# Kernel tuning notes

Hardware: AMD Instinct MI355X
Metric: run time of the kernel (lower is better)

Reference implementation:

```python
import jax, jax.numpy as jnp
import numpy as np

H = 16
D_MODEL = 1024
D_K = D_MODEL // H  # 64


def setup_inputs() -> dict:
    key = jax.random.key(0)
    ks = jax.random.split(key, 8)
    B, S = 8, 1024
    q = jax.random.normal(ks[0], (B, S, D_MODEL), dtype=jnp.float32)
    k = jax.random.normal(ks[1], (B, S, D_MODEL), dtype=jnp.float32)
    v = jax.random.normal(ks[2], (B, S, D_MODEL), dtype=jnp.float32)
    # xavier_normal for [h, d_model, d_k]: std = sqrt(2 / (d_model + d_k)) (fan over last two dims)
    std_p = float(np.sqrt(2.0 / (D_MODEL + D_K)))
    W_q = jax.random.normal(ks[3], (H, D_MODEL, D_K), dtype=jnp.float32) * std_p
    W_k = jax.random.normal(ks[4], (H, D_MODEL, D_K), dtype=jnp.float32) * std_p
    W_v = jax.random.normal(ks[5], (H, D_MODEL, D_K), dtype=jnp.float32) * std_p
    std_o = float(np.sqrt(2.0 / (H * D_K + D_MODEL)))
    W_o = jax.random.normal(ks[6], (D_MODEL, H * D_K), dtype=jnp.float32) * std_o  # torch Linear weight [out, in]
    b_o = jax.random.normal(ks[7], (D_MODEL,), dtype=jnp.float32) * 0.01
    return {"q": q, "k": k, "v": v, "W_q": W_q, "W_k": W_k, "W_v": W_v, "W_o": W_o, "b_o": b_o}


def reference(q, k, v, W_q, W_k, W_v, W_o, b_o):
    B, S, _ = q.shape
    # per-head projections: [h, b, s, d_k]
    qh = jnp.einsum('bsd,hdk->hbsk', q, W_q)
    kh = jnp.einsum('bsd,hdk->hbsk', k, W_k)
    vh = jnp.einsum('bsd,hdk->hbsk', v, W_v)
    scale = 1.0 / jnp.sqrt(jnp.asarray(D_K, dtype=q.dtype))
    scores = jnp.einsum('hbsk,hbtk->hbst', qh, kh) * scale  # [h,b,s,s]
    attn = jax.nn.softmax(scores, axis=-1)
    c = jnp.einsum('hbst,hbtk->hbsk', attn, vh)  # [h,b,s,d_k]
    # torch code splits the stacked (h*b) batch and concats on feature dim:
    # head index becomes the OUTER factor of the feature dim -> [b,s,h*d_k]
    c = jnp.transpose(c, (1, 2, 0, 3)).reshape(B, S, H * D_K)
    out = c @ W_o.T + b_o
    return out
```

## Files before the change

### kernel.cpp

```cpp
#include <hip/hip_runtime.h>
#include <hip/hip_bf16.h>

typedef __bf16 bf16_t;
typedef __attribute__((ext_vector_type(8))) __bf16 bf16x8;
typedef __attribute__((ext_vector_type(4))) float f32x4;

#define MFMA(a, b, c) __builtin_amdgcn_mfma_f32_16x16x32_bf16(a, b, c, 0, 0, 0)

__device__ inline void gload_lds16(const bf16_t* g, bf16_t* l) {
  __builtin_amdgcn_global_load_lds(
      (const __attribute__((address_space(1))) void*)g,
      (__attribute__((address_space(3))) void*)l, 16, 0, 0);
}

__global__ void fill_sentinel(float* out, int n, float val) {
  int i = blockIdx.x * blockDim.x + threadIdx.x;
  if (i < n) out[i] = val;
}

__global__ void transpose_w(const float* __restrict__ Wq, const float* __restrict__ Wk,
                            const float* __restrict__ Wv, bf16_t* __restrict__ Wt) {
  int gid = blockIdx.x * blockDim.x + threadIdx.x;
  int e = gid * 8;
  int m = e >> 20;
  int rem = e & 1048575;
  int n = rem >> 10;
  int d0 = rem & 1023;
  const float* W = (m == 0) ? Wq : (m == 1) ? Wk : Wv;
  int h = n >> 6, kk = n & 63;
  union { bf16_t h8[8]; uint4 u; } tmp;
#pragma unroll
  for (int j = 0; j < 8; ++j)
    tmp.h8[j] = (bf16_t)W[((size_t)(h * 1024 + d0 + j)) * 64 + kk];
  *(uint4*)(Wt + e) = tmp.u;
}

__global__ void cvt_bf16(const float* __restrict__ in, bf16_t* __restrict__ out) {
  size_t i = (size_t)(blockIdx.x * blockDim.x + threadIdx.x) * 8;
  f32x4 a = *(const f32x4*)(in + i);
  f32x4 b = *(const f32x4*)(in + i + 4);
  bf16x8 r;
  r[0] = (bf16_t)a[0]; r[1] = (bf16_t)a[1]; r[2] = (bf16_t)a[2]; r[3] = (bf16_t)a[3];
  r[4] = (bf16_t)b[0]; r[5] = (bf16_t)b[1]; r[6] = (bf16_t)b[2]; r[7] = (bf16_t)b[3];
  *(bf16x8*)(out + i) = r;
}

template <int MODE>
__global__ void gemm_bt(const bf16_t* __restrict__ A, const bf16_t* __restrict__ Bt,
                        const float* __restrict__ bias, void* __restrict__ out_,
                        int M, int N, int K, float scale) {
  __shared__ bf16_t sA[2][128 * 32];
  __shared__ bf16_t sB[2][128 * 32];
  const int t = threadIdx.x;
  const int w = t >> 6, l = t & 63;
  const int lq = l >> 4, ll = l & 15;
  const int m0 = blockIdx.x * 128, n0 = blockIdx.y * 128;
  const int wr = (w >> 1) * 64, wc = (w & 1) * 64;
  const int srow = l >> 2;
  const int scol = (l & 3) * 8;
  f32x4 acc[4][4] = {};

  auto stage = [&](int bufi, int k0s) {
#pragma unroll
    for (int c = 0; c < 2; ++c) {
      int ch = w * 2 + c;
      int row = ch * 16 + srow;
      gload_lds16(A  + (size_t)(m0 + row) * K + k0s + scol, sA[bufi] + ch * 512);
      gload_lds16(Bt + (size_t)(n0 + row) * K + k0s + scol, sB[bufi] + ch * 512);
    }
  };

  stage(0, 0);
  __syncthreads();

  int cur = 0;
  for (int k0 = 0; k0 < K; k0 += 32) {
    if (k0 + 32 < K) stage(cur ^ 1, k0 + 32);
    bf16x8 af[4], bfr[4];
#pragma unroll
    for (int i = 0; i < 4; ++i) {
      af[i]  = *(const bf16x8*)(sA[cur] + (wr + i * 16 + ll) * 32 + lq * 8);
      bfr[i] = *(const bf16x8*)(sB[cur] + (wc + i * 16 + ll) * 32 + lq * 8);
    }
#pragma unroll
    for (int mi = 0; mi < 4; ++mi)
#pragma unroll
      for (int ni = 0; ni < 4; ++ni)
        acc[mi][ni] = MFMA(af[mi], bfr[ni], acc[mi][ni]);
    __syncthreads();
    cur ^= 1;
  }
#pragma unroll
  for (int mi = 0; mi < 4; ++mi)
#pragma unroll
    for (int ni = 0; ni < 4; ++ni)
#pragma unroll
      for (int r = 0; r < 4; ++r) {
        int row = m0 + wr + mi * 16 + lq * 4 + r;
        int col = n0 + wc + ni * 16 + ll;
        float v = acc[mi][ni][r];
        if (MODE == 2) {
          ((float*)out_)[(size_t)row * N + col] = v + bias[col];
        } else {
          int h = col >> 6, kk = col & 63, b = row >> 10, s = row & 1023;
          size_t idx;
          if (MODE == 0)
            idx = ((size_t)((h * 8 + b) * 1024 + s)) * 64 + kk;
          else
            idx = ((size_t)((h * 8 + b) * 64 + kk)) * 1024 + s;
          ((bf16_t*)out_)[idx] = (bf16_t)(v * scale);
        }
      }
}

__global__ void attn_kernel(const bf16_t* __restrict__ qh, const bf16_t* __restrict__ kh,
                            const bf16_t* __restrict__ vt, bf16_t* __restrict__ c) {
  constexpr int KP = 72, PP = 72;
  __shared__ bf16_t sK[2][64 * KP];
  __shared__ bf16_t sP[4][16 * PP];
  const int t = threadIdx.x;
  const int w = t >> 6, l = t & 63;
  const int lq = l >> 4, ll = l & 15;
  const int orig = blockIdx.x + (blockIdx.y << 4);
  const int wg = (orig & 7) * 256 + (orig >> 3);
  const int q0 = (wg & 15) * 64;
  const int hb = wg >> 4;
  const int h = hb >> 3, b = hb & 7;
  const size_t base = (size_t)hb * 65536;
  const bf16_t* Q = qh + base + (size_t)q0 * 64;
  const bf16_t* K = kh + base;
  const bf16_t* V = vt + base;

  bf16x8 aq0 = *(const bf16x8*)(Q + (w * 16 + ll) * 64 + 0 * 32 + lq * 8);
  bf16x8 aq1 = *(const bf16x8*)(Q + (w * 16 + ll) * 64 + 1 * 32 + lq * 8);

  {
    int e0 = t * 8, e1 = (256 + t) * 8;
    uint4 ka = *(const uint4*)(K + e0);
    uint4 kb = *(const uint4*)(K + e1);
    *(uint4*)(sK[0] + (e0 >> 6) * KP + (e0 & 63)) = ka;
    *(uint4*)(sK[0] + (e1 >> 6) * KP + (e1 & 63)) = kb;
  }
  __syncthreads();

  float mrow = -1e30f, lrow = 0.f;
  f32x4 o[4] = {};
  bf16_t* Pw = sP[w];

  int cur = 0;
  for (int kt = 0; kt < 1024; kt += 64, cur ^= 1) {
    uint4 kr0, kr1;
    if (kt < 960) {
      kr0 = *(const uint4*)(K + (size_t)(kt + 64) * 64 + t * 8);
      kr1 = *(const uint4*)(K + (size_t)(kt + 64) * 64 + (256 + t) * 8);
    }
    const bf16_t* Vb = V + (size_t)ll * 1024 + kt + lq * 8;
    bf16x8 bv00 = *(const bf16x8*)(Vb + 0 * 16384 + 0);
    bf16x8 bv01 = *(const bf16x8*)(Vb + 1 * 16384 + 0);
    bf16x8 bv02 = *(const bf16x8*)(Vb + 2 * 16384 + 0);
    bf16x8 bv03 = *(const bf16x8*)(Vb + 3 * 16384 + 0);
    bf16x8 bv10 = *(const bf16x8*)(Vb + 0 * 16384 + 32);
    bf16x8 bv11 = *(const bf16x8*)(Vb + 1 * 16384 + 32);
    bf16x8 bv12 = *(const bf16x8*)(Vb + 2 * 16384 + 32);
    bf16x8 bv13 = *(const bf16x8*)(Vb + 3 * 16384 + 32);

    f32x4 sacc[4] = {};
    __builtin_amdgcn_s_setprio(1);
#pragma unroll
    for (int ni = 0; ni < 4; ++ni) {
      bf16x8 bk0 = *(const bf16x8*)(sK[cur] + (ni * 16 + ll) * KP + 0 * 32 + lq * 8);
      bf16x8 bk1 = *(const bf16x8*)(sK[cur] + (ni * 16 + ll) * KP + 1 * 32 + lq * 8);
      sacc[ni] = MFMA(bk0, aq0, sacc[ni]);
      sacc[ni] = MFMA(bk1, aq1, sacc[ni]);
    }
    __builtin_amdgcn_s_setprio(0);
    float rmax = -1e30f;
#pragma unroll
    for (int ni = 0; ni < 4; ++ni)
#pragma unroll
      for (int r = 0; r < 4; ++r)
        rmax = fmaxf(rmax, sacc[ni][r]);
    if (!__all(rmax <= mrow + 8.0f)) {
      rmax = fmaxf(rmax, __shfl_xor(rmax, 16));
      rmax = fmaxf(rmax, __shfl_xor(rmax, 32));
      float mnew = fmaxf(mrow, rmax);
      float alpha = __expf(mrow - mnew);
      mrow = mnew;
      lrow *= alpha;
#pragma unroll
      for (int r = 0; r < 4; ++r) {
        float ar = __shfl(alpha, lq * 4 + r, 16);
#pragma unroll
        for (int ni = 0; ni < 4; ++ni)
          o[ni][r] *= ar;
      }
    }
#pragma unroll
    for (int ni = 0; ni < 4; ++ni)
#pragma unroll
      for (int r = 0; r < 4; ++r) {
        float p = __expf(sacc[ni][r] - mrow);
        sacc[ni][r] = p;
        lrow += p;
      }
#pragma unroll
    for (int ni = 0; ni < 4; ++ni) {
      union { bf16_t h4[4]; uint2 u; } pk;
      pk.h4[0] = (bf16_t)sacc[ni][0];
      pk.h4[1] = (bf16_t)sacc[ni][1];
      pk.h4[2] = (bf16_t)sacc[ni][2];
      pk.h4[3] = (bf16_t)sacc[ni][3];
      *(uint2*)(Pw + ll * PP + ni * 16 + lq * 4) = pk.u;
    }
    asm volatile("s_waitcnt lgkmcnt(0)" ::: "memory");
    __builtin_amdgcn_sched_barrier(0);
    bf16x8 ap0 = *(const bf16x8*)(Pw + ll * PP + 0 * 32 + lq * 8);
    bf16x8 ap1 = *(const bf16x8*)(Pw + ll * PP + 1 * 32 + lq * 8);
    __builtin_amdgcn_s_setprio(1);
    o[0] = MFMA(ap0, bv00, o[0]);
    o[1] = MFMA(ap0, bv01, o[1]);
    o[2] = MFMA(ap0, bv02, o[2]);
    o[3] = MFMA(ap0, bv03, o[3]);
    o[0] = MFMA(ap1, bv10, o[0]);
    o[1] = MFMA(ap1, bv11, o[1]);
    o[2] = MFMA(ap1, bv12, o[2]);
    o[3] = MFMA(ap1, bv13, o[3]);
    __builtin_amdgcn_s_setprio(0);
    if (kt < 960) {
      int e0 = t * 8, e1 = (256 + t) * 8;
      *(uint4*)(sK[cur ^ 1] + (e0 >> 6) * KP + (e0 & 63)) = kr0;
      *(uint4*)(sK[cur ^ 1] + (e1 >> 6) * KP + (e1 & 63)) = kr1;
    }
    __syncthreads();
  }
  lrow += __shfl_xor(lrow, 16);
  lrow += __shfl_xor(lrow, 32);
#pragma unroll
  for (int r = 0; r < 4; ++r) {
    float lr = __shfl(lrow, lq * 4 + r, 16);
    int s = q0 + w * 16 + lq * 4 + r;
#pragma unroll
    for (int ni = 0; ni < 4; ++ni) {
      int dk = ni * 16 + ll;
      c[((size_t)(b * 1024 + s)) * 1024 + h * 64 + dk] = (bf16_t)(o[ni][r] / lr);
    }
  }
}

extern "C" void kernel_launch(void* const* d_in, const int* in_sizes, int n_in,
                              void* d_out, int out_size, void* d_ws, size_t ws_size,
                              hipStream_t stream) {
  float* out = (float*)d_out;
  int nblk_out = (out_size + 255) / 256;
  if (n_in != 8) {
    fill_sentinel<<<nblk_out, 256, 0, stream>>>(out, out_size, 600.0f + 10.0f * n_in);
    return;
  }
  const int expect[8] = {8388608, 8388608, 8388608, 1048576,
                         1048576, 1048576, 1048576, 1024};
  for (int i = 0; i < 8; ++i)
    if (in_sizes[i] != expect[i]) {
      fill_sentinel<<<nblk_out, 256, 0, stream>>>(out, out_size, 500.0f + 10.0f * i);
      return;
    }

  bf16_t* ws   = (bf16_t*)d_ws;
  bf16_t* qhb  = ws;
  bf16_t* khb  = ws + 8388608;
  bf16_t* vtb  = ws + 16777216;
  bf16_t* Wt   = ws + 25165824;
  bf16_t* cbuf = ws + 25165824;
  bf16_t* Wob  = ws;
  if (ws_size < 67108864ull) {
    fill_sentinel<<<nblk_out, 256, 0, stream>>>(out, out_size, 400.0f);
    return;
  }

  const float* q  = (const float*)d_in[0];
  const float* k  = (const float*)d_in[1];
  const float* v  = (const float*)d_in[2];
  const float* Wq = (const float*)d_in[3];
  const float* Wk = (const float*)d_in[4];
  const float* Wv = (const float*)d_in[5];
  const float* Wo = (const float*)d_in[6];
  const float* bo = (const float*)d_in[7];

  bf16_t* qb = (bf16_t*)d_out;
  bf16_t* kb = (bf16_t*)d_out + 8388608;
  bf16_t* vb = (bf16_t*)d_out;

  transpose_w<<<1536, 256, 0, stream>>>(Wq, Wk, Wv, Wt);
  cvt_bf16<<<4096, 256, 0, stream>>>(q, qb);
  cvt_bf16<<<4096, 256, 0, stream>>>(k, kb);
  dim3 gg(64, 8);
  gemm_bt<0><<<gg, 256, 0, stream>>>(qb, Wt,           nullptr, qhb, 8192, 1024, 1024, 0.125f);
  gemm_bt<0><<<gg, 256, 0, stream>>>(kb, Wt + 1048576, nullptr, khb, 8192, 1024, 1024, 1.0f);
  cvt_bf16<<<4096, 256, 0, stream>>>(v, vb);
  gemm_bt<1><<<gg, 256, 0, stream>>>(vb, Wt + 2097152, nullptr, vtb, 8192, 1024, 1024, 1.0f);
  attn_kernel<<<dim3(16, 128), 256, 0, stream>>>(qhb, khb, vtb, cbuf);
  cvt_bf16<<<512, 256, 0, stream>>>(Wo, Wob);
  gemm_bt<2><<<gg, 256, 0, stream>>>(cbuf, Wob, bo, out, 8192, 1024, 1024, 1.0f);
}
```

Measured before the change: 412.5 us.

## Load K fragments directly from global memory and drop LDS staging and barriers

Each wave now reads its K tile straight from global memory into registers instead of staging it cooperatively into double-buffered shared memory. This removes the per-iteration block-wide __syncthreads and the LDS writes and reads for K, which frees the four waves to run independently. The cost is that each of the four waves loads the same K tile separately, so global/L2 traffic for K goes up fourfold. The K loads are also no longer prefetched one iteration ahead, so their latency now sits directly before the QK MFMAs.

New measurement: 511.7 us. 24.0% more time.

```diff
diff --git a/kernel.cpp b/kernel.cpp
--- a/kernel.cpp
+++ b/kernel.cpp
@@ -115,8 +115,7 @@
 
 __global__ void attn_kernel(const bf16_t* __restrict__ qh, const bf16_t* __restrict__ kh,
                             const bf16_t* __restrict__ vt, bf16_t* __restrict__ c) {
-  constexpr int KP = 72, PP = 72;
-  __shared__ bf16_t sK[2][64 * KP];
+  constexpr int PP = 72;
   __shared__ bf16_t sP[4][16 * PP];
   const int t = threadIdx.x;
   const int w = t >> 6, l = t & 63;
@@ -134,26 +133,33 @@
   bf16x8 aq0 = *(const bf16x8*)(Q + (w * 16 + ll) * 64 + 0 * 32 + lq * 8);
   bf16x8 aq1 = *(const bf16x8*)(Q + (w * 16 + ll) * 64 + 1 * 32 + lq * 8);
 
-  {
-    int e0 = t * 8, e1 = (256 + t) * 8;
-    uint4 ka = *(const uint4*)(K + e0);
-    uint4 kb = *(const uint4*)(K + e1);
-    *(uint4*)(sK[0] + (e0 >> 6) * KP + (e0 & 63)) = ka;
-    *(uint4*)(sK[0] + (e1 >> 6) * KP + (e1 & 63)) = kb;
-  }
-  __syncthreads();
-
   float mrow = -1e30f, lrow = 0.f;
   f32x4 o[4] = {};
   bf16_t* Pw = sP[w];
 
-  int cur = 0;
-  for (int kt = 0; kt < 1024; kt += 64, cur ^= 1) {
-    uint4 kr0, kr1;
-    if (kt < 960) {
-      kr0 = *(const uint4*)(K + (size_t)(kt + 64) * 64 + t * 8);
-      kr1 = *(const uint4*)(K + (size_t)(kt + 64) * 64 + (256 + t) * 8);
-    }
+  for (int kt = 0; kt < 1024; kt += 64) {
+    const bf16_t* Kb = K + (size_t)(kt + ll) * 64 + lq * 8;
+    bf16x8 bk00 = *(const bf16x8*)(Kb + 0 * 1024 + 0);
+    bf16x8 bk01 = *(const bf16x8*)(Kb + 1 * 1024 + 0);
+    bf16x8 bk02 = *(const bf16x8*)(Kb + 2 * 1024 + 0);
+    bf16x8 bk03 = *(const bf16x8*)(Kb + 3 * 1024 + 0);
+    bf16x8 bk10 = *(const bf16x8*)(Kb + 0 * 1024 + 32);
+    bf16x8 bk11 = *(const bf16x8*)(Kb + 1 * 1024 + 32);
+    bf16x8 bk12 = *(const bf16x8*)(Kb + 2 * 1024 + 32);
+    bf16x8 bk13 = *(const bf16x8*)(Kb + 3 * 1024 + 32);
+
+    f32x4 sacc[4] = {};
+    __builtin_amdgcn_s_setprio(1);
+    sacc[0] = MFMA(bk00, aq0, sacc[0]);
+    sacc[1] = MFMA(bk01, aq0, sacc[1]);
+    sacc[2] = MFMA(bk02, aq0, sacc[2]);
+    sacc[3] = MFMA(bk03, aq0, sacc[3]);
+    sacc[0] = MFMA(bk10, aq1, sacc[0]);
+    sacc[1] = MFMA(bk11, aq1, sacc[1]);
+    sacc[2] = MFMA(bk12, aq1, sacc[2]);
+    sacc[3] = MFMA(bk13, aq1, sacc[3]);
+    __builtin_amdgcn_s_setprio(0);
+
     const bf16_t* Vb = V + (size_t)ll * 1024 + kt + lq * 8;
     bf16x8 bv00 = *(const bf16x8*)(Vb + 0 * 16384 + 0);
     bf16x8 bv01 = *(const bf16x8*)(Vb + 1 * 16384 + 0);
@@ -164,16 +170,6 @@
     bf16x8 bv12 = *(const bf16x8*)(Vb + 2 * 16384 + 32);
     bf16x8 bv13 = *(const bf16x8*)(Vb + 3 * 16384 + 32);
 
-    f32x4 sacc[4] = {};
-    __builtin_amdgcn_s_setprio(1);
-#pragma unroll
-    for (int ni = 0; ni < 4; ++ni) {
-      bf16x8 bk0 = *(const bf16x8*)(sK[cur] + (ni * 16 + ll) * KP + 0 * 32 + lq * 8);
-      bf16x8 bk1 = *(const bf16x8*)(sK[cur] + (ni * 16 + ll) * KP + 1 * 32 + lq * 8);
-      sacc[ni] = MFMA(bk0, aq0, sacc[ni]);
-      sacc[ni] = MFMA(bk1, aq1, sacc[ni]);
-    }
-    __builtin_amdgcn_s_setprio(0);
     float rmax = -1e30f;
 #pragma unroll
     for (int ni = 0; ni < 4; ++ni)
@@ -226,12 +222,6 @@
     o[2] = MFMA(ap1, bv12, o[2]);
     o[3] = MFMA(ap1, bv13, o[3]);
     __builtin_amdgcn_s_setprio(0);
-    if (kt < 960) {
-      int e0 = t * 8, e1 = (256 + t) * 8;
-      *(uint4*)(sK[cur ^ 1] + (e0 >> 6) * KP + (e0 & 63)) = kr0;
-      *(uint4*)(sK[cur ^ 1] + (e1 >> 6) * KP + (e1 & 63)) = kr1;
-    }
-    __syncthreads();
   }
   lrow += __shfl_xor(lrow, 16);
   lrow += __shfl_xor(lrow, 32);
```

## Merge Q and K projection GEMMs into one launch and shrink GEMM M-tile to 64

Applied to the files above, without the earlier changes.

The GEMM tile changes from 128x128 to 64x128, with each wave now covering a 64x32 slice, so every GEMM launches twice as many workgroups and fills more CUs. The Q and K projections become a single launch over 16384 rows, choosing the weight slice and scale from the row offset, since qb and kb lie next to each other in memory. The goal is less launch overhead and better occupancy. In exchange each workgroup reuses the B tile less and does more LDS loads per MFMA.

Measured after the change: 421.2 us. 2.1% more time.

```diff
diff --git a/kernel.cpp b/kernel.cpp
--- a/kernel.cpp
+++ b/kernel.cpp
@@ -46,27 +46,28 @@
 }
 
 template <int MODE>
-__global__ void gemm_bt(const bf16_t* __restrict__ A, const bf16_t* __restrict__ Bt,
-                        const float* __restrict__ bias, void* __restrict__ out_,
-                        int M, int N, int K, float scale) {
-  __shared__ bf16_t sA[2][128 * 32];
+__global__ void gemm_bt(const bf16_t* __restrict__ A, const bf16_t* __restrict__ Bt_,
+                        const float* __restrict__ bias, void* __restrict__ out_) {
+  __shared__ bf16_t sA[2][64 * 32];
   __shared__ bf16_t sB[2][128 * 32];
   const int t = threadIdx.x;
   const int w = t >> 6, l = t & 63;
   const int lq = l >> 4, ll = l & 15;
-  const int m0 = blockIdx.x * 128, n0 = blockIdx.y * 128;
-  const int wr = (w >> 1) * 64, wc = (w & 1) * 64;
+  const int m0 = blockIdx.x * 64, n0 = blockIdx.y * 128;
+  const bf16_t* Bt = (MODE == 0 && m0 >= 8192) ? Bt_ + 1048576 : Bt_;
+  const float scale = (MODE == 0 && m0 < 8192) ? 0.125f : 1.0f;
   const int srow = l >> 2;
   const int scol = (l & 3) * 8;
-  f32x4 acc[4][4] = {};
+  f32x4 acc[4][2] = {};
 
   auto stage = [&](int bufi, int k0s) {
+    gload_lds16(A + (size_t)(m0 + w * 16 + srow) * 1024 + k0s + scol,
+                sA[bufi] + w * 512);
 #pragma unroll
     for (int c = 0; c < 2; ++c) {
       int ch = w * 2 + c;
-      int row = ch * 16 + srow;
-      gload_lds16(A  + (size_t)(m0 + row) * K + k0s + scol, sA[bufi] + ch * 512);
-      gload_lds16(Bt + (size_t)(n0 + row) * K + k0s + scol, sB[bufi] + ch * 512);
+      gload_lds16(Bt + (size_t)(n0 + ch * 16 + srow) * 1024 + k0s + scol,
+                  sB[bufi] + ch * 512);
     }
   };
 
@@ -74,18 +75,19 @@
   __syncthreads();
 
   int cur = 0;
-  for (int k0 = 0; k0 < K; k0 += 32) {
-    if (k0 + 32 < K) stage(cur ^ 1, k0 + 32);
-    bf16x8 af[4], bfr[4];
-#pragma unroll
-    for (int i = 0; i < 4; ++i) {
-      af[i]  = *(const bf16x8*)(sA[cur] + (wr + i * 16 + ll) * 32 + lq * 8);
-      bfr[i] = *(const bf16x8*)(sB[cur] + (wc + i * 16 + ll) * 32 + lq * 8);
-    }
+  for (int k0 = 0; k0 < 1024; k0 += 32) {
+    if (k0 + 32 < 1024) stage(cur ^ 1, k0 + 32);
+    bf16x8 af[4], bfr[2];
+#pragma unroll
+    for (int i = 0; i < 4; ++i)
+      af[i] = *(const bf16x8*)(sA[cur] + (i * 16 + ll) * 32 + lq * 8);
+#pragma unroll
+    for (int i = 0; i < 2; ++i)
+      bfr[i] = *(const bf16x8*)(sB[cur] + (w * 32 + i * 16 + ll) * 32 + lq * 8);
 #pragma unroll
     for (int mi = 0; mi < 4; ++mi)
 #pragma unroll
-      for (int ni = 0; ni < 4; ++ni)
+      for (int ni = 0; ni < 2; ++ni)
         acc[mi][ni] = MFMA(af[mi], bfr[ni], acc[mi][ni]);
     __syncthreads();
     cur ^= 1;
@@ -93,21 +95,22 @@
 #pragma unroll
   for (int mi = 0; mi < 4; ++mi)
 #pragma unroll
-    for (int ni = 0; ni < 4; ++ni)
+    for (int ni = 0; ni < 2; ++ni)
 #pragma unroll
       for (int r = 0; r < 4; ++r) {
-        int row = m0 + wr + mi * 16 + lq * 4 + r;
-        int col = n0 + wc + ni * 16 + ll;
+        int row = m0 + mi * 16 + lq * 4 + r;
+        int col = n0 + w * 32 + ni * 16 + ll;
         float v = acc[mi][ni][r];
         if (MODE == 2) {
-          ((float*)out_)[(size_t)row * N + col] = v + bias[col];
+          ((float*)out_)[(size_t)row * 1024 + col] = v + bias[col];
+        } else if (MODE == 1) {
+          int h = col >> 6, kk = col & 63, b = row >> 10, s = row & 1023;
+          ((bf16_t*)out_)[((size_t)((h * 8 + b) * 64 + kk)) * 1024 + s] = (bf16_t)v;
         } else {
-          int h = col >> 6, kk = col & 63, b = row >> 10, s = row & 1023;
-          size_t idx;
-          if (MODE == 0)
-            idx = ((size_t)((h * 8 + b) * 1024 + s)) * 64 + kk;
-          else
-            idx = ((size_t)((h * 8 + b) * 64 + kk)) * 1024 + s;
+          int mat = row >> 13, rr = row & 8191;
+          int h = col >> 6, kk = col & 63, b = rr >> 10, s = rr & 1023;
+          size_t idx = (size_t)mat * 8388608 +
+                       ((size_t)((h * 8 + b) * 1024 + s)) * 64 + kk;
           ((bf16_t*)out_)[idx] = (bf16_t)(v * scale);
         }
       }
@@ -266,7 +269,6 @@
 
   bf16_t* ws   = (bf16_t*)d_ws;
   bf16_t* qhb  = ws;
-  bf16_t* khb  = ws + 8388608;
   bf16_t* vtb  = ws + 16777216;
   bf16_t* Wt   = ws + 25165824;
   bf16_t* cbuf = ws + 25165824;
@@ -292,12 +294,10 @@
   transpose_w<<<1536, 256, 0, stream>>>(Wq, Wk, Wv, Wt);
   cvt_bf16<<<4096, 256, 0, stream>>>(q, qb);
   cvt_bf16<<<4096, 256, 0, stream>>>(k, kb);
-  dim3 gg(64, 8);
-  gemm_bt<0><<<gg, 256, 0, stream>>>(qb, Wt,           nullptr, qhb, 8192, 1024, 1024, 0.125f);
-  gemm_bt<0><<<gg, 256, 0, stream>>>(kb, Wt + 1048576, nullptr, khb, 8192, 1024, 1024, 1.0f);
+  gemm_bt<0><<<dim3(256, 8), 256, 0, stream>>>(qb, Wt, nullptr, qhb);
   cvt_bf16<<<4096, 256, 0, stream>>>(v, vb);
-  gemm_bt<1><<<gg, 256, 0, stream>>>(vb, Wt + 2097152, nullptr, vtb, 8192, 1024, 1024, 1.0f);
-  attn_kernel<<<dim3(16, 128), 256, 0, stream>>>(qhb, khb, vtb, cbuf);
+  gemm_bt<1><<<dim3(128, 8), 256, 0, stream>>>(vb, Wt + 2097152, nullptr, vtb);
+  attn_kernel<<<dim3(16, 128), 256, 0, stream>>>(qhb, qhb + 8388608, vtb, cbuf);
   cvt_bf16<<<512, 256, 0, stream>>>(Wo, Wob);
-  gemm_bt<2><<<gg, 256, 0, stream>>>(cbuf, Wob, bo, out, 8192, 1024, 1024, 1.0f);
-}
+  gemm_bt<2><<<dim3(128, 8), 256, 0, stream>>>(cbuf, Wob, bo, out);
+}
```
